# Performance work log

Hardware: AMD Instinct MI355X
Metric: run time of the kernel (lower is better)

Reference implementation:

```python
import math
import jax, jax.numpy as jnp
import numpy as np


def setup_inputs() -> dict:
    key = jax.random.key(0)
    k1, k2 = jax.random.split(key)
    b, t, h, d = 2, 2048, 16, 64
    q = jax.random.normal(k1, (b, t, h, d), dtype=jnp.float32)
    kv = jax.random.normal(k2, (b, t, 2, h, d), dtype=jnp.float32)
    return {"q": q, "kv": kv}


def reference(q, kv):
    # Padded cross-attention branch, causal=False, dropout=0 (identity).
    d = q.shape[-1]
    softmax_scale = 1.0 / math.sqrt(d)
    k = kv[:, :, 0]  # [b, s, h, d]
    v = kv[:, :, 1]  # [b, s, h, d]
    # scores: [b, h, t, s] -- full score matrix, matching torch einsum
    scores = jnp.einsum('bthd,bshd->bhts', q, k * softmax_scale)
    attention = jax.nn.softmax(scores, axis=-1)
    out = jnp.einsum('bhts,bshd->bthd', attention, v)
    return out
```

## Files before the change

### kernel.cpp

```cpp
#include <hip/hip_runtime.h>
#include <hip/hip_bf16.h>

typedef __attribute__((ext_vector_type(8)))  short v8s;
typedef __attribute__((ext_vector_type(4)))  float v4f;
typedef __attribute__((ext_vector_type(16))) float v16f;
typedef unsigned long long u64;
typedef unsigned short u16;

#define BB 2
#define TT 2048
#define HH 16
#define DD 64


__device__ __forceinline__ unsigned short f2bf(float f) {
    unsigned int u = __builtin_bit_cast(unsigned int, f);
    u = u + 0x7FFFu + ((u >> 16) & 1u);
    return (unsigned short)(u >> 16);
}

__device__ __forceinline__ unsigned cvt2(float a, float b) {
    return ((unsigned)f2bf(b) << 16) | (unsigned)f2bf(a);
}

__device__ __forceinline__ v8s cvt8s(const float4& lo, const float4& hi, float s) {
    union { v8s v; unsigned u[4]; } r;
    r.u[0] = cvt2(lo.x * s, lo.y * s);
    r.u[1] = cvt2(lo.z * s, lo.w * s);
    r.u[2] = cvt2(hi.x * s, hi.y * s);
    r.u[3] = cvt2(hi.z * s, hi.w * s);
    return r.v;
}

__device__ __forceinline__ unsigned cvtpk(float lo, float hi) {
    unsigned r;
    asm("v_cvt_pk_bf16_f32 %0, %1, %2" : "=v"(r) : "v"(lo), "v"(hi));
    return r;
}

__device__ __forceinline__ v8s pack8(u64 lo, u64 hi) {
    union { v8s v; u64 q[2]; } u;
    u.q[0] = lo; u.q[1] = hi;
    return u.v;
}


__global__ __launch_bounds__(256)
void prep_kv(const float* __restrict__ kvg, char* __restrict__ wsi) {
    __shared__ u16 vlds[64][72];
    const int wg  = blockIdx.x;
    const int x   = wg & 7;
    const int rr  = wg >> 3;
    const int p   = x * 4 + (rr & 3);
    const int t64 = rr >> 2;
    const int h   = p & 15;
    const int b   = p >> 4;
    const int t   = threadIdx.x;
    const int s0g = t64 * 64;

    char* obase = wsi + (size_t)p * 524288 + (size_t)t64 * 16384;

    #pragma unroll
    for (int ii = 0; ii < 2; ++ii) {
        int id  = t + 256 * ii;
        int tt2 = id >> 8;
        int al  = (id >> 3) & 31;
        int c   = (id >> 1) & 3;
        int hh  = id & 1;
        const float* kp = kvg + ((((size_t)(b * TT + s0g + 32 * tt2 + al) * 2 + 0) * HH + h) * DD + 16 * c + 4 * hh);
        float4 ka = *(const float4*)kp;
        float4 kb = *(const float4*)(kp + 8);
        *(v8s*)(obase + tt2 * 8192 + c * 1024 + (((hh << 5) | al) << 4)) = cvt8s(ka, kb, 1.0f);
    }
    #pragma unroll
    for (int ii = 0; ii < 2; ++ii) {
        int id  = t + 256 * ii;
        int row = id >> 3;
        int d8  = id & 7;
        const float* vp = kvg + ((((size_t)(b * TT + s0g + row) * 2 + 1) * HH + h) * DD + 8 * d8);
        float4 va = *(const float4*)vp;
        float4 vb = *(const float4*)(vp + 4);
        *(v8s*)&vlds[row][8 * d8] = cvt8s(va, vb, 1.0f);
    }
    __syncthreads();
    #pragma unroll
    for (int ii = 0; ii < 2; ++ii) {
        int id  = t + 256 * ii;
        int tt2 = id >> 8;
        int k   = (id >> 6) & 3;
        int l   = id & 63;
        int dt  = k >> 1, cc = k & 1;
        int al  = l & 31, hh = l >> 5;
        union { v8s v; u16 w[8]; } r;
        #pragma unroll
        for (int j = 0; j < 4; ++j) {
            r.w[j]     = vlds[32 * tt2 + 16 * cc + 4 * hh + j][32 * dt + al];
            r.w[4 + j] = vlds[32 * tt2 + 16 * cc + 8 + 4 * hh + j][32 * dt + al];
        }
        *(v8s*)(obase + tt2 * 8192 + 4096 + k * 1024 + (l << 4)) = r.v;
    }
}


__global__ __launch_bounds__(256, 3)
void attn_v7(const float* __restrict__ qg, const char* __restrict__ wsi,
             float* __restrict__ outg) {
    __shared__ float mg[2][64][34];

    const int bid  = blockIdx.x;
    const int wgid = (bid & 7) * 128 + (bid >> 3);
    const int qb   = wgid & 31;
    const int hH   = (wgid >> 5) & 15;
    const int b    = wgid >> 9;
    const int tid  = threadIdx.x;
    const int lane = tid & 63;
    const int w    = tid >> 6;
    const int qh   = w & 1;
    const int g    = w >> 1;
    const int al   = lane & 31;
    const int hh   = lane >> 5;

    const char* kvb = wsi + (size_t)(b * 16 + hH) * 524288 + (size_t)g * 262144;

    const int q0 = qb * 64 + qh * 32;
    const int qr = q0 + al;

    const float qscale = 0.125f * 1.4426950408889634f;
    v8s qf[4];
    {
        const float* qp = qg + ((size_t)((b * TT + qr) * HH + hH)) * DD;
        #pragma unroll
        for (int c = 0; c < 4; ++c) {
            float4 lo = *(const float4*)(qp + 16 * c + 4 * hh);
            float4 hi = *(const float4*)(qp + 16 * c + 4 * hh + 8);
            qf[c] = cvt8s(lo, hi, qscale);
        }
    }

#define LOADK(dst, ii)                                                        \
    do {                                                                      \
        const char* tb_ = kvb + (size_t)(ii) * 8192 + (size_t)lane * 16;      \
        dst[0] = *(const v8s*)(tb_);                                          \
        dst[1] = *(const v8s*)(tb_ + 1024);                                   \
        dst[2] = *(const v8s*)(tb_ + 2048);                                   \
        dst[3] = *(const v8s*)(tb_ + 3072);                                   \
    } while (0)
#define LOADV(dst, ii)                                                        \
    do {                                                                      \
        const char* tb_ = kvb + (size_t)(ii) * 8192 + 4096 + (size_t)lane * 16; \
        dst[0] = *(const v8s*)(tb_);                                          \
        dst[1] = *(const v8s*)(tb_ + 1024);                                   \
        dst[2] = *(const v8s*)(tb_ + 2048);                                   \
        dst[3] = *(const v8s*)(tb_ + 3072);                                   \
    } while (0)

    v8s kf[4], kn[4], vf[4];
    LOADK(kf, 0);

    v16f oa[2];
    #pragma unroll
    for (int dt = 0; dt < 2; ++dt)
        #pragma unroll
        for (int r = 0; r < 16; ++r) oa[dt][r] = 0.0f;
    float m = -INFINITY, lsum = 0.0f;

    #pragma unroll 2
    for (int i = 0; i < 32; ++i) {
        LOADV(vf, i);
        if (i < 31) LOADK(kn, i + 1);

        v16f st;
        #pragma unroll
        for (int r = 0; r < 16; ++r) st[r] = 0.0f;
        __builtin_amdgcn_s_setprio(1);
        #pragma unroll
        for (int c = 0; c < 4; ++c)
            st = __builtin_amdgcn_mfma_f32_32x32x16_bf16(kf[c], qf[c], st, 0, 0, 0);
        __builtin_amdgcn_s_setprio(0);

        float mc = st[0];
        #pragma unroll
        for (int r = 1; r < 16; ++r) mc = fmaxf(mc, st[r]);
        mc = fmaxf(mc, __shfl_xor(mc, 32));
        if (!__all(mc - m <= 8.0f)) {
            float mnew  = fmaxf(m, mc);
            float alpha = __builtin_amdgcn_exp2f(m - mnew);
            lsum *= alpha;
            m = mnew;
            #pragma unroll
            for (int dt = 0; dt < 2; ++dt)
                #pragma unroll
                for (int r = 0; r < 16; ++r) oa[dt][r] *= alpha;
        }
        float ps = 0.0f;
        #pragma unroll
        for (int r = 0; r < 16; ++r) {
            float e = __builtin_amdgcn_exp2f(st[r] - m);
            st[r] = e;
            ps += e;
        }
        ps += __shfl_xor(ps, 32);
        lsum += ps;

        v8s pf[2];
        #pragma unroll
        for (int cc = 0; cc < 2; ++cc) {
            union { v8s v; unsigned u[4]; } r;
            #pragma unroll
            for (int ww = 0; ww < 4; ++ww)
                r.u[ww] = cvtpk(st[8 * cc + 2 * ww], st[8 * cc + 2 * ww + 1]);
            pf[cc] = r.v;
        }

        __builtin_amdgcn_s_setprio(1);
        #pragma unroll
        for (int cc = 0; cc < 2; ++cc)
            #pragma unroll
            for (int dt = 0; dt < 2; ++dt)
                oa[dt] = __builtin_amdgcn_mfma_f32_32x32x16_bf16(vf[dt * 2 + cc], pf[cc], oa[dt], 0, 0, 0);
        __builtin_amdgcn_s_setprio(0);

        #pragma unroll
        for (int c = 0; c < 4; ++c) kf[c] = kn[c];
    }

    __syncthreads();
    if (g == 1) {
        float* p = &mg[qh][lane & 63][0];
        #pragma unroll
        for (int dt = 0; dt < 2; ++dt)
            #pragma unroll
            for (int r = 0; r < 16; ++r) p[dt * 16 + r] = oa[dt][r];
        p[32] = m;
        p[33] = lsum;
    }
    __syncthreads();
    if (g == 0) {
        const float* p = &mg[qh][lane & 63][0];
        float m1 = p[32], l1 = p[33];
        float ms = fmaxf(m, m1);
        float a0 = __builtin_amdgcn_exp2f(m - ms);
        float a1 = __builtin_amdgcn_exp2f(m1 - ms);
        float li = 1.0f / (lsum * a0 + l1 * a1);
        const size_t obase = ((size_t)((b * TT + qr) * HH + hH)) * DD;
        #pragma unroll
        for (int dt = 0; dt < 2; ++dt)
            #pragma unroll
            for (int r = 0; r < 16; ++r) {
                int d = 32 * dt + (r & 3) + 8 * (r >> 2) + 4 * hh;
                outg[obase + d] = (oa[dt][r] * a0 + p[dt * 16 + r] * a1) * li;
            }
    }
}


__global__ __launch_bounds__(256)
void attn_fwd_v1(const float* __restrict__ qg, const float* __restrict__ kvg,
                 float* __restrict__ outg) {
    __shared__ __align__(16) u16 Klds[32][68];
    __shared__ __align__(16) u16 Vt[DD][36];

    const int wg    = blockIdx.x;
    const int qtile = wg & 31;
    const int h     = (wg >> 5) & 15;
    const int b     = wg >> 9;
    const int tid   = threadIdx.x;
    const int lane  = tid & 63;
    const int wid   = tid >> 6;
    const int lr    = lane & 15;
    const int lg    = lane >> 4;
    const int q0    = qtile * 64 + wid * 16;

    const float qscale = 0.125f * 1.4426950408889634f;
    v8s qf[2];
    {
        const float* qb = qg + ((size_t)((b * TT + q0 + lr) * HH + h)) * DD;
        #pragma unroll
        for (int c = 0; c < 2; ++c) {
            float4 lo = *(const float4*)(qb + 32 * c + 4 * lg);
            float4 hi = *(const float4*)(qb + 32 * c + 4 * lg + 16);
            qf[c] = cvt8s(lo, hi, qscale);
        }
    }

    v4f oa[4];
    #pragma unroll
    for (int dc = 0; dc < 4; ++dc)
        #pragma unroll
        for (int r = 0; r < 4; ++r) oa[dc][r] = 0.0f;
    float m = -INFINITY, lsum = 0.0f;

    for (int kv0 = 0; kv0 < TT; kv0 += 32) {
        __syncthreads();
        #pragma unroll
        for (int i = 0; i < 2; ++i) {
            int id  = tid + 256 * i;
            int row = id >> 4;
            int cg  = (id & 15) * 4;
            const float* gp = kvg + ((size_t)(((b * TT + kv0 + row) * 2 + 0) * HH + h)) * DD + cg;
            float4 f = *(const float4*)gp;
            ushort4 w;
            w.x = f2bf(f.x); w.y = f2bf(f.y); w.z = f2bf(f.z); w.w = f2bf(f.w);
            *(ushort4*)&Klds[row][cg] = w;
        }
        {
            int s0 = tid >> 4;
            int dg = (tid & 15) * 4;
            const float* gp0 = kvg + ((size_t)(((b * TT + kv0 + 2 * s0) * 2 + 1) * HH + h)) * DD + dg;
            const float* gp1 = gp0 + 2 * HH * DD;
            float4 fa = *(const float4*)gp0;
            float4 fb = *(const float4*)gp1;
            float av[4] = {fa.x, fa.y, fa.z, fa.w};
            float bv[4] = {fb.x, fb.y, fb.z, fb.w};
            #pragma unroll
            for (int i = 0; i < 4; ++i) {
                ushort2 w;
                w.x = f2bf(av[i]);
                w.y = f2bf(bv[i]);
                *(ushort2*)&Vt[dg + i][2 * s0] = w;
            }
        }
        __syncthreads();

        v4f st0, st1;
        #pragma unroll
        for (int r = 0; r < 4; ++r) { st0[r] = 0.0f; st1[r] = 0.0f; }
        #pragma unroll
        for (int c = 0; c < 2; ++c) {
            {
                u64 lo = *(const u64*)&Klds[lr][32 * c + 4 * lg];
                u64 hi = *(const u64*)&Klds[lr][32 * c + 4 * lg + 16];
                st0 = __builtin_amdgcn_mfma_f32_16x16x32_bf16(pack8(lo, hi), qf[c], st0, 0, 0, 0);
            }
            {
                u64 lo = *(const u64*)&Klds[16 + lr][32 * c + 4 * lg];
                u64 hi = *(const u64*)&Klds[16 + lr][32 * c + 4 * lg + 16];
                st1 = __builtin_amdgcn_mfma_f32_16x16x32_bf16(pack8(lo, hi), qf[c], st1, 0, 0, 0);
            }
        }

        float sc[8] = {st0[0], st0[1], st0[2], st0[3], st1[0], st1[1], st1[2], st1[3]};
        float mc = sc[0];
        #pragma unroll
        for (int i = 1; i < 8; ++i) mc = fmaxf(mc, sc[i]);
        mc = fmaxf(mc, __shfl_xor(mc, 16));
        mc = fmaxf(mc, __shfl_xor(mc, 32));
        float mnew  = fmaxf(m, mc);
        float alpha = __builtin_amdgcn_exp2f(m - mnew);
        float p[8], ps = 0.0f;
        #pragma unroll
        for (int i = 0; i < 8; ++i) { p[i] = __builtin_amdgcn_exp2f(sc[i] - mnew); ps += p[i]; }
        ps += __shfl_xor(ps, 16);
        ps += __shfl_xor(ps, 32);
        lsum = lsum * alpha + ps;
        m = mnew;

        float ar0 = __shfl(alpha, 4 * lg + 0);
        float ar1 = __shfl(alpha, 4 * lg + 1);
        float ar2 = __shfl(alpha, 4 * lg + 2);
        float ar3 = __shfl(alpha, 4 * lg + 3);
        #pragma unroll
        for (int dc = 0; dc < 4; ++dc) {
            oa[dc][0] *= ar0; oa[dc][1] *= ar1; oa[dc][2] *= ar2; oa[dc][3] *= ar3;
        }

        v8s pf;
        #pragma unroll
        for (int i = 0; i < 8; ++i) pf[i] = (short)f2bf(p[i]);

        #pragma unroll
        for (int dc = 0; dc < 4; ++dc) {
            u64 lo = *(const u64*)&Vt[16 * dc + lr][4 * lg];
            u64 hi = *(const u64*)&Vt[16 * dc + lr][4 * lg + 16];
            oa[dc] = __builtin_amdgcn_mfma_f32_16x16x32_bf16(pf, pack8(lo, hi), oa[dc], 0, 0, 0);
        }
    }

    float rl  = 1.0f / lsum;
    float rr0 = __shfl(rl, 4 * lg + 0);
    float rr1 = __shfl(rl, 4 * lg + 1);
    float rr2 = __shfl(rl, 4 * lg + 2);
    float rr3 = __shfl(rl, 4 * lg + 3);
    #pragma unroll
    for (int dc = 0; dc < 4; ++dc) {
        size_t base = ((size_t)((b * TT + q0) * HH + h)) * DD + 16 * dc + lr;
        outg[base + (size_t)(4 * lg + 0) * HH * DD] = oa[dc][0] * rr0;
        outg[base + (size_t)(4 * lg + 1) * HH * DD] = oa[dc][1] * rr1;
        outg[base + (size_t)(4 * lg + 2) * HH * DD] = oa[dc][2] * rr2;
        outg[base + (size_t)(4 * lg + 3) * HH * DD] = oa[dc][3] * rr3;
    }
}

extern "C" void kernel_launch(void* const* d_in, const int* in_sizes, int n_in,
                              void* d_out, int out_size, void* d_ws, size_t ws_size,
                              hipStream_t stream) {
    const float* q  = (const float*)d_in[0];
    const float* kv = (const float*)d_in[1];
    float* out      = (float*)d_out;
    if (ws_size >= (size_t)16777216) {
        char* wsi = (char*)d_ws;
        hipLaunchKernelGGL(prep_kv, dim3(1024), dim3(256), 0, stream, kv, wsi);
        hipLaunchKernelGGL(attn_v7, dim3(1024), dim3(256), 0, stream, q, wsi, out);
    } else {
        hipLaunchKernelGGL(attn_fwd_v1, dim3(1024), dim3(256), 0, stream, q, kv, out);
    }
}
```

Measured before the change: 64.60 us.

## Process two query subtiles per wave to reuse K/V fragments across 128-row blocks

```diff
diff --git a/kernel.cpp b/kernel.cpp
--- a/kernel.cpp
+++ b/kernel.cpp
@@ -102,16 +102,17 @@
 }
 
 
-__global__ __launch_bounds__(256, 3)
-void attn_v7(const float* __restrict__ qg, const char* __restrict__ wsi,
+__global__ __launch_bounds__(256, 2)
+void attn_v8(const float* __restrict__ qg, const char* __restrict__ wsi,
              float* __restrict__ outg) {
-    __shared__ float mg[2][64][34];
+    __shared__ float mg[2][2][64][34];
 
     const int bid  = blockIdx.x;
-    const int wgid = (bid & 7) * 128 + (bid >> 3);
-    const int qb   = wgid & 31;
-    const int hH   = (wgid >> 5) & 15;
-    const int b    = wgid >> 9;
+    const int wgid = (bid & 7) * 64 + (bid >> 3);
+    const int qb   = wgid & 15;
+    const int p    = wgid >> 4;
+    const int hH   = p & 15;
+    const int b    = p >> 4;
     const int tid  = threadIdx.x;
     const int lane = tid & 63;
     const int w    = tid >> 6;
@@ -120,136 +121,163 @@
     const int al   = lane & 31;
     const int hh   = lane >> 5;
 
-    const char* kvb = wsi + (size_t)(b * 16 + hH) * 524288 + (size_t)g * 262144;
-
-    const int q0 = qb * 64 + qh * 32;
-    const int qr = q0 + al;
+    const char* kvb = wsi + (size_t)p * 524288 + (size_t)g * 262144;
+    const int q0 = qb * 128 + qh * 64;
 
     const float qscale = 0.125f * 1.4426950408889634f;
-    v8s qf[4];
-    {
-        const float* qp = qg + ((size_t)((b * TT + qr) * HH + hH)) * DD;
+    v8s qf[2][4];
+    #pragma unroll
+    for (int s = 0; s < 2; ++s) {
+        const float* qp = qg + ((size_t)((b * TT + q0 + 32 * s + al) * HH + hH)) * DD;
         #pragma unroll
         for (int c = 0; c < 4; ++c) {
             float4 lo = *(const float4*)(qp + 16 * c + 4 * hh);
             float4 hi = *(const float4*)(qp + 16 * c + 4 * hh + 8);
-            qf[c] = cvt8s(lo, hi, qscale);
-        }
-    }
-
-#define LOADK(dst, ii)                                                        \
-    do {                                                                      \
-        const char* tb_ = kvb + (size_t)(ii) * 8192 + (size_t)lane * 16;      \
-        dst[0] = *(const v8s*)(tb_);                                          \
-        dst[1] = *(const v8s*)(tb_ + 1024);                                   \
-        dst[2] = *(const v8s*)(tb_ + 2048);                                   \
-        dst[3] = *(const v8s*)(tb_ + 3072);                                   \
+            qf[s][c] = cvt8s(lo, hi, qscale);
+        }
+    }
+
+#define LOADK8(dst, ii)                                                         \
+    do {                                                                        \
+        const char* tb_ = kvb + (size_t)(ii) * 8192 + (size_t)lane * 16;        \
+        dst[0] = *(const v8s*)(tb_);                                            \
+        dst[1] = *(const v8s*)(tb_ + 1024);                                     \
+        dst[2] = *(const v8s*)(tb_ + 2048);                                     \
+        dst[3] = *(const v8s*)(tb_ + 3072);                                     \
     } while (0)
-#define LOADV(dst, ii)                                                        \
-    do {                                                                      \
+#define LOADV8(dst, ii)                                                         \
+    do {                                                                        \
         const char* tb_ = kvb + (size_t)(ii) * 8192 + 4096 + (size_t)lane * 16; \
-        dst[0] = *(const v8s*)(tb_);                                          \
-        dst[1] = *(const v8s*)(tb_ + 1024);                                   \
-        dst[2] = *(const v8s*)(tb_ + 2048);                                   \
-        dst[3] = *(const v8s*)(tb_ + 3072);                                   \
+        dst[0] = *(const v8s*)(tb_);                                            \
+        dst[1] = *(const v8s*)(tb_ + 1024);                                     \
+        dst[2] = *(const v8s*)(tb_ + 2048);                                     \
+        dst[3] = *(const v8s*)(tb_ + 3072);                                     \
     } while (0)
 
-    v8s kf[4], kn[4], vf[4];
-    LOADK(kf, 0);
-
-    v16f oa[2];
-    #pragma unroll
-    for (int dt = 0; dt < 2; ++dt)
-        #pragma unroll
-        for (int r = 0; r < 16; ++r) oa[dt][r] = 0.0f;
-    float m = -INFINITY, lsum = 0.0f;
-
-    #pragma unroll 2
-    for (int i = 0; i < 32; ++i) {
-        LOADV(vf, i);
-        if (i < 31) LOADK(kn, i + 1);
-
-        v16f st;
-        #pragma unroll
-        for (int r = 0; r < 16; ++r) st[r] = 0.0f;
-        __builtin_amdgcn_s_setprio(1);
-        #pragma unroll
-        for (int c = 0; c < 4; ++c)
-            st = __builtin_amdgcn_mfma_f32_32x32x16_bf16(kf[c], qf[c], st, 0, 0, 0);
-        __builtin_amdgcn_s_setprio(0);
-
-        float mc = st[0];
-        #pragma unroll
-        for (int r = 1; r < 16; ++r) mc = fmaxf(mc, st[r]);
-        mc = fmaxf(mc, __shfl_xor(mc, 32));
-        if (!__all(mc - m <= 8.0f)) {
-            float mnew  = fmaxf(m, mc);
-            float alpha = __builtin_amdgcn_exp2f(m - mnew);
-            lsum *= alpha;
-            m = mnew;
+    v8s kfA[4], kfB[4], vfA[4], vfB[4];
+
+    v16f oa[2][2];
+    #pragma unroll
+    for (int s = 0; s < 2; ++s)
+        #pragma unroll
+        for (int dt = 0; dt < 2; ++dt)
+            #pragma unroll
+            for (int r = 0; r < 16; ++r) oa[s][dt][r] = 0.0f;
+    float m[2]    = {-INFINITY, -INFINITY};
+    float lsum[2] = {0.0f, 0.0f};
+
+    auto body = [&](const v8s (&kf)[4], const v8s (&vf)[4]) {
+        v16f st[2];
+        #pragma unroll
+        for (int s = 0; s < 2; ++s)
+            #pragma unroll
+            for (int r = 0; r < 16; ++r) st[s][r] = 0.0f;
+        #pragma unroll
+        for (int c = 0; c < 4; ++c) {
+            st[0] = __builtin_amdgcn_mfma_f32_32x32x16_bf16(kf[c], qf[0][c], st[0], 0, 0, 0);
+            st[1] = __builtin_amdgcn_mfma_f32_32x32x16_bf16(kf[c], qf[1][c], st[1], 0, 0, 0);
+        }
+
+        float mc[2];
+        #pragma unroll
+        for (int s = 0; s < 2; ++s) {
+            float t0 = fmaxf(st[s][0], st[s][1]),   t1 = fmaxf(st[s][2], st[s][3]);
+            float t2 = fmaxf(st[s][4], st[s][5]),   t3 = fmaxf(st[s][6], st[s][7]);
+            float t4 = fmaxf(st[s][8], st[s][9]),   t5 = fmaxf(st[s][10], st[s][11]);
+            float t6 = fmaxf(st[s][12], st[s][13]), t7 = fmaxf(st[s][14], st[s][15]);
+            t0 = fmaxf(t0, t1); t2 = fmaxf(t2, t3); t4 = fmaxf(t4, t5); t6 = fmaxf(t6, t7);
+            mc[s] = fmaxf(fmaxf(t0, t2), fmaxf(t4, t6));
+        }
+        bool trig = (mc[0] - m[0] > 8.0f) || (mc[1] - m[1] > 8.0f);
+        if (__any(trig)) {
+            #pragma unroll
+            for (int s = 0; s < 2; ++s) {
+                float rm    = fmaxf(mc[s], __shfl_xor(mc[s], 32));
+                float mnew  = fmaxf(m[s], rm);
+                float alpha = __builtin_amdgcn_exp2f(m[s] - mnew);
+                lsum[s] *= alpha;
+                m[s] = mnew;
+                #pragma unroll
+                for (int dt = 0; dt < 2; ++dt)
+                    #pragma unroll
+                    for (int r = 0; r < 16; ++r) oa[s][dt][r] *= alpha;
+            }
+        }
+
+        #pragma unroll
+        for (int s = 0; s < 2; ++s) {
+            #pragma unroll
+            for (int r = 0; r < 16; ++r)
+                st[s][r] = __builtin_amdgcn_exp2f(st[s][r] - m[s]);
+            float a0 = st[s][0] + st[s][1],   a1 = st[s][2] + st[s][3];
+            float a2 = st[s][4] + st[s][5],   a3 = st[s][6] + st[s][7];
+            float a4 = st[s][8] + st[s][9],   a5 = st[s][10] + st[s][11];
+            float a6 = st[s][12] + st[s][13], a7 = st[s][14] + st[s][15];
+            a0 += a1; a2 += a3; a4 += a5; a6 += a7;
+            lsum[s] += (a0 + a2) + (a4 + a6);
+
+            v8s pf[2];
+            #pragma unroll
+            for (int cc = 0; cc < 2; ++cc) {
+                union { v8s v; unsigned u[4]; } r;
+                #pragma unroll
+                for (int ww = 0; ww < 4; ++ww)
+                    r.u[ww] = cvtpk(st[s][8 * cc + 2 * ww], st[s][8 * cc + 2 * ww + 1]);
+                pf[cc] = r.v;
+            }
+            #pragma unroll
+            for (int cc = 0; cc < 2; ++cc)
+                #pragma unroll
+                for (int dt = 0; dt < 2; ++dt)
+                    oa[s][dt] = __builtin_amdgcn_mfma_f32_32x32x16_bf16(vf[dt * 2 + cc], pf[cc], oa[s][dt], 0, 0, 0);
+        }
+    };
+
+    LOADK8(kfA, 0);
+    for (int i = 0; i < 32; i += 2) {
+        LOADV8(vfA, i);
+        LOADK8(kfB, i + 1);
+        LOADV8(vfB, i + 1);
+        body(kfA, vfA);
+        if (i + 2 < 32) LOADK8(kfA, i + 2);
+        body(kfB, vfB);
+    }
+
+    #pragma unroll
+    for (int s = 0; s < 2; ++s) lsum[s] += __shfl_xor(lsum[s], 32);
+
+    __syncthreads();
+    if (g == 1) {
+        #pragma unroll
+        for (int s = 0; s < 2; ++s) {
+            float* pp = &mg[qh][s][lane][0];
             #pragma unroll
             for (int dt = 0; dt < 2; ++dt)
                 #pragma unroll
-                for (int r = 0; r < 16; ++r) oa[dt][r] *= alpha;
-        }
-        float ps = 0.0f;
-        #pragma unroll
-        for (int r = 0; r < 16; ++r) {
-            float e = __builtin_amdgcn_exp2f(st[r] - m);
-            st[r] = e;
-            ps += e;
-        }
-        ps += __shfl_xor(ps, 32);
-        lsum += ps;
-
-        v8s pf[2];
-        #pragma unroll
-        for (int cc = 0; cc < 2; ++cc) {
-            union { v8s v; unsigned u[4]; } r;
-            #pragma unroll
-            for (int ww = 0; ww < 4; ++ww)
-                r.u[ww] = cvtpk(st[8 * cc + 2 * ww], st[8 * cc + 2 * ww + 1]);
-            pf[cc] = r.v;
-        }
-
-        __builtin_amdgcn_s_setprio(1);
-        #pragma unroll
-        for (int cc = 0; cc < 2; ++cc)
-            #pragma unroll
-            for (int dt = 0; dt < 2; ++dt)
-                oa[dt] = __builtin_amdgcn_mfma_f32_32x32x16_bf16(vf[dt * 2 + cc], pf[cc], oa[dt], 0, 0, 0);
-        __builtin_amdgcn_s_setprio(0);
-
-        #pragma unroll
-        for (int c = 0; c < 4; ++c) kf[c] = kn[c];
-    }
-
-    __syncthreads();
-    if (g == 1) {
-        float* p = &mg[qh][lane & 63][0];
-        #pragma unroll
-        for (int dt = 0; dt < 2; ++dt)
-            #pragma unroll
-            for (int r = 0; r < 16; ++r) p[dt * 16 + r] = oa[dt][r];
-        p[32] = m;
-        p[33] = lsum;
+                for (int r = 0; r < 16; ++r) pp[dt * 16 + r] = oa[s][dt][r];
+            pp[32] = m[s];
+            pp[33] = lsum[s];
+        }
     }
     __syncthreads();
     if (g == 0) {
-        const float* p = &mg[qh][lane & 63][0];
-        float m1 = p[32], l1 = p[33];
-        float ms = fmaxf(m, m1);
-        float a0 = __builtin_amdgcn_exp2f(m - ms);
-        float a1 = __builtin_amdgcn_exp2f(m1 - ms);
-        float li = 1.0f / (lsum * a0 + l1 * a1);
-        const size_t obase = ((size_t)((b * TT + qr) * HH + hH)) * DD;
-        #pragma unroll
-        for (int dt = 0; dt < 2; ++dt)
-            #pragma unroll
-            for (int r = 0; r < 16; ++r) {
-                int d = 32 * dt + (r & 3) + 8 * (r >> 2) + 4 * hh;
-                outg[obase + d] = (oa[dt][r] * a0 + p[dt * 16 + r] * a1) * li;
-            }
+        #pragma unroll
+        for (int s = 0; s < 2; ++s) {
+            const float* pp = &mg[qh][s][lane][0];
+            float m1 = pp[32], l1 = pp[33];
+            float ms = fmaxf(m[s], m1);
+            float a0 = __builtin_amdgcn_exp2f(m[s] - ms);
+            float a1 = __builtin_amdgcn_exp2f(m1 - ms);
+            float li = 1.0f / (lsum[s] * a0 + l1 * a1);
+            const size_t obase = ((size_t)((b * TT + q0 + 32 * s + al) * HH + hH)) * DD;
+            #pragma unroll
+            for (int dt = 0; dt < 2; ++dt)
+                #pragma unroll
+                for (int r = 0; r < 16; ++r) {
+                    int d = 32 * dt + (r & 3) + 8 * (r >> 2) + 4 * hh;
+                    outg[obase + d] = (oa[s][dt][r] * a0 + pp[dt * 16 + r] * a1) * li;
+                }
+        }
     }
 }
 
@@ -400,7 +428,7 @@
     if (ws_size >= (size_t)16777216) {
         char* wsi = (char*)d_ws;
         hipLaunchKernelGGL(prep_kv, dim3(1024), dim3(256), 0, stream, kv, wsi);
-        hipLaunchKernelGGL(attn_v7, dim3(1024), dim3(256), 0, stream, q, wsi, out);
+        hipLaunchKernelGGL(attn_v8, dim3(512), dim3(256), 0, stream, q, wsi, out);
     } else {
         hipLaunchKernelGGL(attn_fwd_v1, dim3(1024), dim3(256), 0, stream, q, kv, out);
     }
```

Result: faster. 58.81 us (-9.0%).
